# Kernel optimization log

Measured on AMD Instinct MI355X. Metric: run time of the kernel, lower is better.

## Reference

```python
import jax, jax.numpy as jnp
import numpy as np

D0 = 232          # GraphSAGE_TextMF_dyn.model_embedding_dim_origin
NUM_TRAIN = 4096  # num_train_models


def sage_conv(x, edge_index, W_l, b_l, W_r):
    """PyG SAGEConv(aggr='mean'): lin_l(mean_{j in N(i)} x_j) + lin_r(x_i)."""
    src, dst = edge_index[0], edge_index[1]
    msg = x[src]                                                    # [E, Din]
    agg = jax.ops.segment_sum(msg, dst, num_segments=x.shape[0])    # [N, Din]
    deg = jax.ops.segment_sum(jnp.ones((edge_index.shape[1],), x.dtype), dst,
                              num_segments=x.shape[0])
    agg = agg / jnp.maximum(deg, 1.0)[:, None]
    return agg @ W_l.T + b_l + x @ W_r.T


def setup_inputs() -> dict:
    key = jax.random.key(0)
    ks = jax.random.split(key, 12)
    num_models, med, hidden = 5000, 1024, 256
    num_prompts, text_dim = 100000, 768
    B, E = 16384, 131072
    s = lambda d: 1.0 / np.sqrt(d)
    return {
        "P_weight":     jax.random.normal(ks[0], (num_models, med), jnp.float32) * 0.02,
        "model_proj_W": jax.random.normal(ks[1], (D0, med), jnp.float32) * s(med),
        "model_proj_b": jnp.zeros((D0,), jnp.float32),
        "sage1_Wl":     jax.random.normal(ks[2], (hidden, D0), jnp.float32) * s(D0),
        "sage1_bl":     jnp.zeros((hidden,), jnp.float32),
        "sage1_Wr":     jax.random.normal(ks[3], (hidden, D0), jnp.float32) * s(D0),
        "sage2_Wl":     jax.random.normal(ks[4], (D0, hidden), jnp.float32) * s(hidden),
        "sage2_bl":     jnp.zeros((D0,), jnp.float32),
        "sage2_Wr":     jax.random.normal(ks[5], (D0, hidden), jnp.float32) * s(hidden),
        "Q_weight":     jax.random.normal(ks[6], (num_prompts, text_dim), jnp.float32),
        "text_proj_W":  jax.random.normal(ks[7], (D0, text_dim), jnp.float32) * s(text_dim),
        "text_proj_b":  jnp.zeros((D0,), jnp.float32),
        "cls_W":        jax.random.normal(ks[8], (2, D0), jnp.float32) * s(D0),
        "cls_b":        jnp.zeros((2,), jnp.float32),
        "edge_index":   jax.random.randint(ks[9], (2, E), 0, NUM_TRAIN),
        "model_ids":    jax.random.randint(ks[10], (B,), 0, NUM_TRAIN),
        "prompt_ids":   jax.random.randint(ks[11], (B,), 0, num_prompts),
    }


def reference(P_weight, model_proj_W, model_proj_b,
              sage1_Wl, sage1_bl, sage1_Wr,
              sage2_Wl, sage2_bl, sage2_Wr,
              Q_weight, text_proj_W, text_proj_b,
              cls_W, cls_b,
              edge_index, model_ids, prompt_ids):
    # model embedding table -> project to D0
    emb = P_weight @ model_proj_W.T + model_proj_b            # [num_models, D0]
    x = emb[:NUM_TRAIN]                                       # train models only
    # 2-layer GraphSAGE with ReLU between layers
    x = jax.nn.relu(sage_conv(x, edge_index, sage1_Wl, sage1_bl, sage1_Wr))
    x = sage_conv(x, edge_index, sage2_Wl, sage2_bl, sage2_Wr)  # [NUM_TRAIN, D0]
    # TextMF head: classifier(p * q)
    p = x[model_ids]                                          # [B, D0]
    q = Q_weight[prompt_ids] @ text_proj_W.T + text_proj_b    # [B, D0]
    return (p * q) @ cls_W.T + cls_b                          # [B, 2]
```

## Files before the change

### kernel.cpp

```cpp
#include <hip/hip_runtime.h>

#define D0 232
#define MED 1024
#define HID 256
#define TDIM 768
#define NTRAIN 4096

typedef short bf16x8 __attribute__((ext_vector_type(8)));
typedef float f32x4  __attribute__((ext_vector_type(4)));
typedef unsigned short u16;

__device__ __forceinline__ u16 f2bf(float f) {
    unsigned u = __float_as_uint(f);
    return (u16)((u + 0x7FFFu + ((u >> 16) & 1u)) >> 16);
}
__device__ __forceinline__ float bf2f(u16 h) {
    return __uint_as_float(((unsigned)h) << 16);
}
__device__ __forceinline__ void cvt8(const float4& a0, const float4& a1,
                                     bf16x8& h, bf16x8& l) {
    float f[8] = {a0.x, a0.y, a0.z, a0.w, a1.x, a1.y, a1.z, a1.w};
    #pragma unroll
    for (int i = 0; i < 8; ++i) {
        u16 hh = f2bf(f[i]);
        h[i] = (short)hh;
        l[i] = (short)f2bf(f[i] - bf2f(hh));
    }
}

#define SROW(r, k) ((((r) ^ (k)) & 7) | ((r) & ~7))

template<int RELU, int EMIT>
__global__ __launch_bounds__(256) void gemm_node(
    const float* __restrict__ A1,
    const short* __restrict__ Whi, const short* __restrict__ Wlo,
    const short* __restrict__ A2hi, const short* __restrict__ A2lo,
    const short* __restrict__ W2hi, const short* __restrict__ W2lo,
    const float* __restrict__ bias,
    float* __restrict__ Cf, u16* __restrict__ Chi, u16* __restrict__ Clo,
    int M, int N, int K)
{
    constexpr int TBM = 32, TBN = 128;
    __shared__ short sAh[8 * TBM * 8], sAl[8 * TBM * 8];
    __shared__ short sBh[8 * TBN * 8], sBl[8 * TBN * 8];

    const int tid  = threadIdx.x;
    const int lane = tid & 63;
    const int wn   = tid >> 6;
    const int l15  = lane & 15;
    const int l4   = lane >> 4;
    const int row0 = blockIdx.y * TBM;
    const int col0 = blockIdx.x * TBN;

    const int aRow  = tid >> 3;
    const int aKc   = tid & 7;
    const int aSlot = (aKc * TBM + SROW(aRow, aKc)) * 8;

    int bKcA[4], bSlot[4], bRowL[4];
    #pragma unroll
    for (int i = 0; i < 4; ++i) {
        int cid  = tid * 4 + i;
        bRowL[i] = cid >> 3;
        bKcA[i]  = cid & 7;
        bSlot[i] = (bKcA[i] * TBN + SROW(bRowL[i], bKcA[i])) * 8;
    }

    const bf16x8 Z8 = {0, 0, 0, 0, 0, 0, 0, 0};
    f32x4 acc[2][2];
    #pragma unroll
    for (int m = 0; m < 2; ++m)
        #pragma unroll
        for (int j = 0; j < 2; ++j)
            acc[m][j] = (f32x4){0.f, 0.f, 0.f, 0.f};

    for (int pass = 0; pass < 2; ++pass) {
        if (pass && A2hi == nullptr) break;
        const short* Bh = pass ? W2hi : Whi;
        const short* Bl = pass ? W2lo : Wlo;

        const size_t aBase = (size_t)(row0 + aRow) * K;
        size_t bBase[4]; bool bOk[4];
        #pragma unroll
        for (int i = 0; i < 4; ++i) {
            int c = col0 + bRowL[i];
            bOk[i]   = c < N;
            bBase[i] = (size_t)(bOk[i] ? c : 0) * K;
        }

        float4 a0, a1;
        bf16x8 pAh, pAl, rBh[4], rBl[4];

        auto loadT = [&](int k0) {
            int gk = k0 + aKc * 8;
            bool av = gk < K;
            if (pass == 0) {
                a0 = av ? *reinterpret_cast<const float4*>(A1 + aBase + gk)
                        : make_float4(0.f, 0.f, 0.f, 0.f);
                a1 = av ? *reinterpret_cast<const float4*>(A1 + aBase + gk + 4)
                        : make_float4(0.f, 0.f, 0.f, 0.f);
            } else {
                pAh = av ? *reinterpret_cast<const bf16x8*>(A2hi + aBase + gk) : Z8;
                pAl = av ? *reinterpret_cast<const bf16x8*>(A2lo + aBase + gk) : Z8;
            }
            #pragma unroll
            for (int i = 0; i < 4; ++i) {
                int k = k0 + bKcA[i] * 8;
                bool v = bOk[i] && k < K;
                rBh[i] = v ? *reinterpret_cast<const bf16x8*>(Bh + bBase[i] + k) : Z8;
                rBl[i] = v ? *reinterpret_cast<const bf16x8*>(Bl + bBase[i] + k) : Z8;
            }
        };
        auto storeT = [&]() {
            if (pass == 0) {
                bf16x8 h, l; cvt8(a0, a1, h, l);
                *reinterpret_cast<bf16x8*>(sAh + aSlot) = h;
                *reinterpret_cast<bf16x8*>(sAl + aSlot) = l;
            } else {
                *reinterpret_cast<bf16x8*>(sAh + aSlot) = pAh;
                *reinterpret_cast<bf16x8*>(sAl + aSlot) = pAl;
            }
            #pragma unroll
            for (int i = 0; i < 4; ++i) {
                *reinterpret_cast<bf16x8*>(sBh + bSlot[i]) = rBh[i];
                *reinterpret_cast<bf16x8*>(sBl + bSlot[i]) = rBl[i];
            }
        };

        loadT(0);
        for (int k0 = 0; k0 < K; k0 += 64) {
            storeT();
            __syncthreads();
            if (k0 + 64 < K) loadT(k0 + 64);
            #pragma unroll
            for (int ks = 0; ks < 2; ++ks) {
                const int pb = ks * 4 + l4;
                bf16x8 ah[2], al[2], bh[2], bl[2];
                #pragma unroll
                for (int m = 0; m < 2; ++m) {
                    int r  = m * 16 + l15;
                    int sl = (pb * TBM + SROW(r, pb)) * 8;
                    ah[m] = *reinterpret_cast<const bf16x8*>(sAh + sl);
                    al[m] = *reinterpret_cast<const bf16x8*>(sAl + sl);
                }
                #pragma unroll
                for (int j = 0; j < 2; ++j) {
                    int r  = wn * 32 + j * 16 + l15;
                    int sl = (pb * TBN + SROW(r, pb)) * 8;
                    bh[j] = *reinterpret_cast<const bf16x8*>(sBh + sl);
                    bl[j] = *reinterpret_cast<const bf16x8*>(sBl + sl);
                }
                #pragma unroll
                for (int m = 0; m < 2; ++m)
                    #pragma unroll
                    for (int j = 0; j < 2; ++j)
                        acc[m][j] = __builtin_amdgcn_mfma_f32_16x16x32_bf16(
                            ah[m], bh[j], acc[m][j], 0, 0, 0);
                #pragma unroll
                for (int m = 0; m < 2; ++m)
                    #pragma unroll
                    for (int j = 0; j < 2; ++j)
                        acc[m][j] = __builtin_amdgcn_mfma_f32_16x16x32_bf16(
                            ah[m], bl[j], acc[m][j], 0, 0, 0);
                #pragma unroll
                for (int m = 0; m < 2; ++m)
                    #pragma unroll
                    for (int j = 0; j < 2; ++j)
                        acc[m][j] = __builtin_amdgcn_mfma_f32_16x16x32_bf16(
                            al[m], bh[j], acc[m][j], 0, 0, 0);
            }
            __syncthreads();
        }
    }

    #pragma unroll
    for (int j = 0; j < 2; ++j) {
        int col = col0 + wn * 32 + j * 16 + l15;
        if (col >= N) continue;
        float bv = bias[col];
        #pragma unroll
        for (int m = 0; m < 2; ++m) {
            #pragma unroll
            for (int r = 0; r < 4; ++r) {
                int row = row0 + m * 16 + l4 * 4 + r;
                float v = acc[m][j][r] + bv;
                if (RELU) v = fmaxf(v, 0.0f);
                size_t idx = (size_t)row * N + col;
                Cf[idx] = v;
                if (EMIT) {
                    u16 h = f2bf(v);
                    Chi[idx] = h;
                    Clo[idx] = f2bf(v - bf2f(h));
                }
            }
        }
    }
}

__global__ __launch_bounds__(512) void gemm_q_head(
    const float* __restrict__ Q,
    const int* __restrict__ prompt_ids,
    const short* __restrict__ Whi, const short* __restrict__ Wlo,
    const float* __restrict__ bias,
    const float* __restrict__ x2f,
    const int* __restrict__ model_ids,
    const float* __restrict__ cls_W, const float* __restrict__ cls_b,
    float* __restrict__ out)
{
    constexpr int TBM = 64, TBN = 256, K = TDIM, N = D0;
    __shared__ short sAh[8 * TBM * 8], sAl[8 * TBM * 8];
    __shared__ short sBh[8 * TBN * 8], sBl[8 * TBN * 8];
    __shared__ float hacc[TBM][2];

    const int tid  = threadIdx.x;
    const int lane = tid & 63;
    const int wave = tid >> 6;
    const int wm   = wave >> 2;
    const int wn   = wave & 3;
    const int l15  = lane & 15;
    const int l4   = lane >> 4;
    const int row0 = blockIdx.x * TBM;

    const int aRow  = tid >> 3;
    const int aKc   = tid & 7;
    const int aSlot = (aKc * TBM + SROW(aRow, aKc)) * 8;
    const size_t aBase = (size_t)prompt_ids[row0 + aRow] * K;

    int bKcA[4], bSlot[4]; bool bOk[4]; size_t bBase[4];
    #pragma unroll
    for (int i = 0; i < 4; ++i) {
        int cid   = tid * 4 + i;
        int br    = cid >> 3;
        bKcA[i]   = cid & 7;
        bSlot[i]  = (bKcA[i] * TBN + SROW(br, bKcA[i])) * 8;
        bOk[i]    = br < N;
        bBase[i]  = (size_t)(bOk[i] ? br : 0) * K;
    }

    const bf16x8 Z8 = {0, 0, 0, 0, 0, 0, 0, 0};
    f32x4 acc[2][4];
    #pragma unroll
    for (int m = 0; m < 2; ++m)
        #pragma unroll
        for (int j = 0; j < 4; ++j)
            acc[m][j] = (f32x4){0.f, 0.f, 0.f, 0.f};

    float4 a0, a1;
    bf16x8 rBh[4], rBl[4];

    auto loadT = [&](int k0) {
        int gk = k0 + aKc * 8;
        a0 = *reinterpret_cast<const float4*>(Q + aBase + gk);
        a1 = *reinterpret_cast<const float4*>(Q + aBase + gk + 4);
        #pragma unroll
        for (int i = 0; i < 4; ++i) {
            int k = k0 + bKcA[i] * 8;
            rBh[i] = bOk[i] ? *reinterpret_cast<const bf16x8*>(Whi + bBase[i] + k) : Z8;
            rBl[i] = bOk[i] ? *reinterpret_cast<const bf16x8*>(Wlo + bBase[i] + k) : Z8;
        }
    };
    auto storeT = [&]() {
        bf16x8 h, l; cvt8(a0, a1, h, l);
        *reinterpret_cast<bf16x8*>(sAh + aSlot) = h;
        *reinterpret_cast<bf16x8*>(sAl + aSlot) = l;
        #pragma unroll
        for (int i = 0; i < 4; ++i) {
            *reinterpret_cast<bf16x8*>(sBh + bSlot[i]) = rBh[i];
            *reinterpret_cast<bf16x8*>(sBl + bSlot[i]) = rBl[i];
        }
    };

    loadT(0);
    for (int k0 = 0; k0 < K; k0 += 64) {
        storeT();
        __syncthreads();
        if (k0 + 64 < K) loadT(k0 + 64);
        #pragma unroll
        for (int ks = 0; ks < 2; ++ks) {
            const int pb = ks * 4 + l4;
            bf16x8 ah[2], al[2], bh[4], bl[4];
            #pragma unroll
            for (int m = 0; m < 2; ++m) {
                int r  = wm * 32 + m * 16 + l15;
                int sl = (pb * TBM + SROW(r, pb)) * 8;
                ah[m] = *reinterpret_cast<const bf16x8*>(sAh + sl);
                al[m] = *reinterpret_cast<const bf16x8*>(sAl + sl);
            }
            #pragma unroll
            for (int j = 0; j < 4; ++j) {
                int r  = wn * 64 + j * 16 + l15;
                int sl = (pb * TBN + SROW(r, pb)) * 8;
                bh[j] = *reinterpret_cast<const bf16x8*>(sBh + sl);
                bl[j] = *reinterpret_cast<const bf16x8*>(sBl + sl);
            }
            #pragma unroll
            for (int m = 0; m < 2; ++m)
                #pragma unroll
                for (int j = 0; j < 4; ++j)
                    acc[m][j] = __builtin_amdgcn_mfma_f32_16x16x32_bf16(
                        ah[m], bh[j], acc[m][j], 0, 0, 0);
            #pragma unroll
            for (int m = 0; m < 2; ++m)
                #pragma unroll
                for (int j = 0; j < 4; ++j)
                    acc[m][j] = __builtin_amdgcn_mfma_f32_16x16x32_bf16(
                        ah[m], bl[j], acc[m][j], 0, 0, 0);
            #pragma unroll
            for (int m = 0; m < 2; ++m)
                #pragma unroll
                for (int j = 0; j < 4; ++j)
                    acc[m][j] = __builtin_amdgcn_mfma_f32_16x16x32_bf16(
                        al[m], bh[j], acc[m][j], 0, 0, 0);
        }
        __syncthreads();
    }

    for (int t = tid; t < TBM * 2; t += 512) ((float*)hacc)[t] = 0.f;
    __syncthreads();

    int mids[2][4];
    #pragma unroll
    for (int m = 0; m < 2; ++m)
        #pragma unroll
        for (int rr = 0; rr < 4; ++rr)
            mids[m][rr] = model_ids[row0 + wm * 32 + m * 16 + l4 * 4 + rr];

    float s[2][4][2] = {};
    #pragma unroll
    for (int j = 0; j < 4; ++j) {
        int col = wn * 64 + j * 16 + l15;
        if (col < N) {
            float w0 = cls_W[col], w1 = cls_W[N + col], bv = bias[col];
            #pragma unroll
            for (int m = 0; m < 2; ++m) {
                #pragma unroll
                for (int rr = 0; rr < 4; ++rr) {
                    float p  = x2f[(size_t)mids[m][rr] * N + col];
                    float pv = (acc[m][j][rr] + bv) * p;
                    s[m][rr][0] += pv * w0;
                    s[m][rr][1] += pv * w1;
                }
            }
        }
    }
    #pragma unroll
    for (int off = 1; off < 16; off <<= 1)
        #pragma unroll
        for (int m = 0; m < 2; ++m)
            #pragma unroll
            for (int rr = 0; rr < 4; ++rr) {
                s[m][rr][0] += __shfl_xor(s[m][rr][0], off);
                s[m][rr][1] += __shfl_xor(s[m][rr][1], off);
            }
    if (l15 == 0) {
        #pragma unroll
        for (int m = 0; m < 2; ++m)
            #pragma unroll
            for (int rr = 0; rr < 4; ++rr) {
                int lr = wm * 32 + m * 16 + l4 * 4 + rr;
                atomicAdd(&hacc[lr][0], s[m][rr][0]);
                atomicAdd(&hacc[lr][1], s[m][rr][1]);
            }
    }
    __syncthreads();
    for (int t = tid; t < TBM; t += 512) {
        out[(size_t)(row0 + t) * 2 + 0] = hacc[t][0] + cls_b[0];
        out[(size_t)(row0 + t) * 2 + 1] = hacc[t][1] + cls_b[1];
    }
}

struct Seg  { const float* src; u16* hi; u16* lo; int n4; };
struct Segs { Seg s[6]; };

__global__ __launch_bounds__(256) void conv_multi(Segs segs, int total4)
{
    int i = blockIdx.x * blockDim.x + threadIdx.x;
    const int stride = gridDim.x * blockDim.x;
    for (; i < total4; i += stride) {
        int k = i, si = 0;
        while (k >= segs.s[si].n4) { k -= segs.s[si].n4; ++si; }
        float4 v = reinterpret_cast<const float4*>(segs.s[si].src)[k];
        float f[4] = {v.x, v.y, v.z, v.w};
        ushort4 h, l;
        u16* hp = (u16*)&h; u16* lp = (u16*)&l;
        #pragma unroll
        for (int c = 0; c < 4; ++c) {
            u16 hh = f2bf(f[c]);
            hp[c] = hh; lp[c] = f2bf(f[c] - bf2f(hh));
        }
        reinterpret_cast<ushort4*>(segs.s[si].hi)[k] = h;
        reinterpret_cast<ushort4*>(segs.s[si].lo)[k] = l;
    }
}

__global__ void hist_kernel(const int* __restrict__ dst, int* __restrict__ hist, int E)
{
    int e = blockIdx.x * blockDim.x + threadIdx.x;
    if (e < E) atomicAdd(&hist[dst[e]], 1);
}

__global__ __launch_bounds__(1024) void scan_kernel(
    const int* __restrict__ hist, int* __restrict__ row_ptr,
    float* __restrict__ invdeg, int E)
{
    __shared__ int s[1024];
    const int t = threadIdx.x;
    int4 c = reinterpret_cast<const int4*>(hist)[t];
    int local = c.x + c.y + c.z + c.w;
    s[t] = local;
    __syncthreads();
    for (int off = 1; off < 1024; off <<= 1) {
        int v = (t >= off) ? s[t - off] : 0;
        __syncthreads();
        s[t] += v;
        __syncthreads();
    }
    int base = s[t] - local;
    row_ptr[4 * t + 0] = base;
    row_ptr[4 * t + 1] = base + c.x;
    row_ptr[4 * t + 2] = base + c.x + c.y;
    row_ptr[4 * t + 3] = base + c.x + c.y + c.z;
    if (t == 1023) row_ptr[4096] = E;
    invdeg[4 * t + 0] = 1.0f / fmaxf((float)c.x, 1.0f);
    invdeg[4 * t + 1] = 1.0f / fmaxf((float)c.y, 1.0f);
    invdeg[4 * t + 2] = 1.0f / fmaxf((float)c.z, 1.0f);
    invdeg[4 * t + 3] = 1.0f / fmaxf((float)c.w, 1.0f);
}

__global__ void scatter_kernel(
    const int* __restrict__ src, const int* __restrict__ dst,
    const int* __restrict__ row_ptr, int* __restrict__ cursor,
    int* __restrict__ csr, int E)
{
    int e = blockIdx.x * blockDim.x + threadIdx.x;
    if (e >= E) return;
    int d = dst[e];
    int pos = atomicAdd(&cursor[d], 1);
    csr[row_ptr[d] + pos] = src[e];
}

__device__ __forceinline__ void add4(float4& a, const float4 b) {
    a.x += b.x; a.y += b.y; a.z += b.z; a.w += b.w;
}

__global__ __launch_bounds__(256) void node_agg(
    const int* __restrict__ row_ptr, const int* __restrict__ csr,
    const float* __restrict__ invdeg,
    const float* __restrict__ x, float* __restrict__ agg, int D)
{
    const int wave = threadIdx.x >> 6;
    const int lane = threadIdx.x & 63;
    const int node = blockIdx.x * 4 + wave;
    const int beg = row_ptr[node], end = row_ptr[node + 1];
    const bool act = lane < (D >> 2);
    const int fo = lane * 4;

    float4 s0 = {0,0,0,0}, s1 = {0,0,0,0}, s2 = {0,0,0,0}, s3 = {0,0,0,0};
    int j = beg;
    for (; j + 3 < end; j += 4) {
        int n0 = csr[j], n1 = csr[j + 1], n2 = csr[j + 2], n3 = csr[j + 3];
        if (act) {
            add4(s0, *reinterpret_cast<const float4*>(&x[(size_t)n0 * D + fo]));
            add4(s1, *reinterpret_cast<const float4*>(&x[(size_t)n1 * D + fo]));
            add4(s2, *reinterpret_cast<const float4*>(&x[(size_t)n2 * D + fo]));
            add4(s3, *reinterpret_cast<const float4*>(&x[(size_t)n3 * D + fo]));
        }
    }
    for (; j < end; ++j) {
        int n = csr[j];
        if (act) add4(s0, *reinterpret_cast<const float4*>(&x[(size_t)n * D + fo]));
    }
    if (act) {
        const float inv = invdeg[node];
        float4 r;
        r.x = (s0.x + s1.x + s2.x + s3.x) * inv;
        r.y = (s0.y + s1.y + s2.y + s3.y) * inv;
        r.z = (s0.z + s1.z + s2.z + s3.z) * inv;
        r.w = (s0.w + s1.w + s2.w + s3.w) * inv;
        *reinterpret_cast<float4*>(&agg[(size_t)node * D + fo]) = r;
    }
}

extern "C" void kernel_launch(void* const* d_in, const int* in_sizes, int n_in,
                              void* d_out, int out_size, void* d_ws, size_t ws_size,
                              hipStream_t stream)
{
    const float* P_weight     = (const float*)d_in[0];
    const float* model_proj_W = (const float*)d_in[1];
    const float* model_proj_b = (const float*)d_in[2];
    const float* sage1_Wl     = (const float*)d_in[3];
    const float* sage1_bl     = (const float*)d_in[4];
    const float* sage1_Wr     = (const float*)d_in[5];
    const float* sage2_Wl     = (const float*)d_in[6];
    const float* sage2_bl     = (const float*)d_in[7];
    const float* sage2_Wr     = (const float*)d_in[8];
    const float* Q_weight     = (const float*)d_in[9];
    const float* text_proj_W  = (const float*)d_in[10];
    const float* text_proj_b  = (const float*)d_in[11];
    const float* cls_W        = (const float*)d_in[12];
    const float* cls_b        = (const float*)d_in[13];
    const int*   edge_index   = (const int*)d_in[14];
    const int*   model_ids    = (const int*)d_in[15];
    const int*   prompt_ids   = (const int*)d_in[16];

    const int E = in_sizes[14] / 2;
    const int B = in_sizes[15];
    const int* srcE = edge_index;
    const int* dstE = edge_index + E;

    const size_t nX0 = (size_t)NTRAIN * D0;
    const size_t nH1 = (size_t)NTRAIN * HID;
    const size_t nWp = (size_t)D0 * MED;
    const size_t nWs = (size_t)HID * D0;
    const size_t nWt = (size_t)D0 * TDIM;
    const size_t nWAll = nWp + 4 * nWs + nWt;

    float* fp  = (float*)d_ws;
    float* x0f = fp;  fp += nX0;
    float* h1f = fp;  fp += nH1;
    float* x2f = fp;  fp += nX0;
    float* agf = fp;  fp += nH1;
    u16* sp  = (u16*)fp;
    u16* x0h = sp;    sp += nX0;
    u16* x0l = sp;    sp += nX0;
    u16* h1h = sp;    sp += nH1;
    u16* h1l = sp;    sp += nH1;
    u16* Wh  = sp;    sp += nWAll;
    u16* Wl  = sp;    sp += nWAll;
    int* ib  = (int*)sp;
    int*   hist    = ib;
    int*   cursor  = ib + 4096;
    int*   row_ptr = ib + 8192;
    float* invdeg  = (float*)(ib + 12304);
    int*   csr     = ib + 16400;

    u16 *Wph = Wh,            *Wpl = Wl;
    u16 *W1lh = Wh + nWp,     *W1ll = Wl + nWp;
    u16 *W1rh = W1lh + nWs,   *W1rl = W1ll + nWs;
    u16 *W2lh = W1rh + nWs,   *W2ll = W1rl + nWs;
    u16 *W2rh = W2lh + nWs,   *W2rl = W2ll + nWs;
    u16 *Wth  = W2rh + nWs,   *Wtl  = W2rl + nWs;

    dim3 blk(256);

    hipMemsetAsync(ib, 0, 8192 * sizeof(int), stream);

    hist_kernel<<<(E + 255) / 256, blk, 0, stream>>>(dstE, hist, E);
    scan_kernel<<<1, 1024, 0, stream>>>(hist, row_ptr, invdeg, E);
    scatter_kernel<<<(E + 255) / 256, blk, 0, stream>>>(srcE, dstE, row_ptr, cursor, csr, E);

    Segs segs;
    segs.s[0] = {model_proj_W, Wph,  Wpl,  (int)(nWp / 4)};
    segs.s[1] = {sage1_Wl,     W1lh, W1ll, (int)(nWs / 4)};
    segs.s[2] = {sage1_Wr,     W1rh, W1rl, (int)(nWs / 4)};
    segs.s[3] = {sage2_Wl,     W2lh, W2ll, (int)(nWs / 4)};
    segs.s[4] = {sage2_Wr,     W2rh, W2rl, (int)(nWs / 4)};
    segs.s[5] = {text_proj_W,  Wth,  Wtl,  (int)(nWt / 4)};
    conv_multi<<<640, blk, 0, stream>>>(segs, (int)(nWAll / 4));

    gemm_node<0, 1><<<dim3(2, NTRAIN / 32), blk, 0, stream>>>(
        P_weight, (const short*)Wph, (const short*)Wpl,
        nullptr, nullptr, nullptr, nullptr,
        model_proj_b, x0f, x0h, x0l, NTRAIN, D0, MED);

    node_agg<<<NTRAIN / 4, blk, 0, stream>>>(row_ptr, csr, invdeg, x0f, agf, D0);

    gemm_node<1, 1><<<dim3(2, NTRAIN / 32), blk, 0, stream>>>(
        agf, (const short*)W1lh, (const short*)W1ll,
        (const short*)x0h, (const short*)x0l,
        (const short*)W1rh, (const short*)W1rl,
        sage1_bl, h1f, h1h, h1l, NTRAIN, HID, D0);

    node_agg<<<NTRAIN / 4, blk, 0, stream>>>(row_ptr, csr, invdeg, h1f, agf, HID);

    gemm_node<0, 0><<<dim3(2, NTRAIN / 32), blk, 0, stream>>>(
        agf, (const short*)W2lh, (const short*)W2ll,
        (const short*)h1h, (const short*)h1l,
        (const short*)W2rh, (const short*)W2rl,
        sage2_bl, x2f, nullptr, nullptr, NTRAIN, D0, HID);

    gemm_q_head<<<B / 64, dim3(512), 0, stream>>>(
        Q_weight, prompt_ids, (const short*)Wth, (const short*)Wtl,
        text_proj_b, x2f, model_ids, cls_W, cls_b, (float*)d_out);
}
```

Baseline: 167.8 us.

## Load GEMM weight fragments directly into registers, fuse hist with weight conversion

The node GEMMs and the Q-head GEMM no longer stage the weight (B) tiles in shared memory. Each wave now loads its bf16 hi/lo weight fragments straight from global memory into registers. The node GEMM tile narrows to 64 columns with more blocks and a 2-blocks-per-CU launch bound, and the Q-head moves to 256 threads with each wave covering all 64 rows. The histogram kernel is merged with the weight-conversion kernel, the cursor memset moves into the scan, and node_agg writes bf16 hi/lo splits directly so the next GEMM skips its conversion. This removes launches, LDS traffic and syncs, at the cost of redundant global weight reads across row blocks and more register pressure.

```diff
diff --git a/kernel.cpp b/kernel.cpp
--- a/kernel.cpp
+++ b/kernel.cpp
@@ -27,22 +27,28 @@
         l[i] = (short)f2bf(f[i] - bf2f(hh));
     }
 }
+__device__ __forceinline__ void cvt4(const float4 v, ushort4& h, ushort4& l) {
+    h.x = f2bf(v.x); l.x = f2bf(v.x - bf2f(h.x));
+    h.y = f2bf(v.y); l.y = f2bf(v.y - bf2f(h.y));
+    h.z = f2bf(v.z); l.z = f2bf(v.z - bf2f(h.z));
+    h.w = f2bf(v.w); l.w = f2bf(v.w - bf2f(h.w));
+}
 
 #define SROW(r, k) ((((r) ^ (k)) & 7) | ((r) & ~7))
 
-template<int RELU, int EMIT>
-__global__ __launch_bounds__(256) void gemm_node(
-    const float* __restrict__ A1,
-    const short* __restrict__ Whi, const short* __restrict__ Wlo,
-    const short* __restrict__ A2hi, const short* __restrict__ A2lo,
-    const short* __restrict__ W2hi, const short* __restrict__ W2lo,
+template<int CONVA, int RELU, int EMIT, int NPASS>
+__global__ __launch_bounds__(256, 2) void gemm_node(
+    const float* __restrict__ A1f,
+    const short* __restrict__ A1h, const short* __restrict__ A1l,
+    const short* __restrict__ B1h, const short* __restrict__ B1l,
+    const short* __restrict__ A2h, const short* __restrict__ A2l,
+    const short* __restrict__ B2h, const short* __restrict__ B2l,
     const float* __restrict__ bias,
     float* __restrict__ Cf, u16* __restrict__ Chi, u16* __restrict__ Clo,
     int M, int N, int K)
 {
-    constexpr int TBM = 32, TBN = 128;
+    constexpr int TBM = 32;
     __shared__ short sAh[8 * TBM * 8], sAl[8 * TBM * 8];
-    __shared__ short sBh[8 * TBN * 8], sBl[8 * TBN * 8];
 
     const int tid  = threadIdx.x;
     const int lane = tid & 63;
@@ -50,141 +56,98 @@
     const int l15  = lane & 15;
     const int l4   = lane >> 4;
     const int row0 = blockIdx.y * TBM;
-    const int col0 = blockIdx.x * TBN;
+    const int col0 = blockIdx.x * 64;
 
     const int aRow  = tid >> 3;
     const int aKc   = tid & 7;
     const int aSlot = (aKc * TBM + SROW(aRow, aKc)) * 8;
 
-    int bKcA[4], bSlot[4], bRowL[4];
-    #pragma unroll
-    for (int i = 0; i < 4; ++i) {
-        int cid  = tid * 4 + i;
-        bRowL[i] = cid >> 3;
-        bKcA[i]  = cid & 7;
-        bSlot[i] = (bKcA[i] * TBN + SROW(bRowL[i], bKcA[i])) * 8;
-    }
+    const int  colW  = col0 + wn * 16 + l15;
+    const bool colOk = colW < N;
+    const size_t wBase = (size_t)(colOk ? colW : 0) * K;
 
     const bf16x8 Z8 = {0, 0, 0, 0, 0, 0, 0, 0};
-    f32x4 acc[2][2];
-    #pragma unroll
-    for (int m = 0; m < 2; ++m)
-        #pragma unroll
-        for (int j = 0; j < 2; ++j)
-            acc[m][j] = (f32x4){0.f, 0.f, 0.f, 0.f};
-
-    for (int pass = 0; pass < 2; ++pass) {
-        if (pass && A2hi == nullptr) break;
-        const short* Bh = pass ? W2hi : Whi;
-        const short* Bl = pass ? W2lo : Wlo;
-
-        const size_t aBase = (size_t)(row0 + aRow) * K;
-        size_t bBase[4]; bool bOk[4];
-        #pragma unroll
-        for (int i = 0; i < 4; ++i) {
-            int c = col0 + bRowL[i];
-            bOk[i]   = c < N;
-            bBase[i] = (size_t)(bOk[i] ? c : 0) * K;
-        }
-
-        float4 a0, a1;
-        bf16x8 pAh, pAl, rBh[4], rBl[4];
-
-        auto loadT = [&](int k0) {
+    f32x4 acc[2];
+    acc[0] = (f32x4){0.f, 0.f, 0.f, 0.f};
+    acc[1] = (f32x4){0.f, 0.f, 0.f, 0.f};
+
+    for (int pass = 0; pass < NPASS; ++pass) {
+        const short* Bh = pass ? B2h : B1h;
+        const short* Bl = pass ? B2l : B1l;
+        const short* Ah = pass ? A2h : A1h;
+        const short* Al = pass ? A2l : A1l;
+        const size_t aOff = (size_t)(row0 + aRow) * K;
+
+        float4 qa0, qa1;
+        bf16x8 ph, pl;
+
+        auto loadA = [&](int k0) {
             int gk = k0 + aKc * 8;
-            bool av = gk < K;
-            if (pass == 0) {
-                a0 = av ? *reinterpret_cast<const float4*>(A1 + aBase + gk)
-                        : make_float4(0.f, 0.f, 0.f, 0.f);
-                a1 = av ? *reinterpret_cast<const float4*>(A1 + aBase + gk + 4)
-                        : make_float4(0.f, 0.f, 0.f, 0.f);
+            bool v = gk < K;
+            if (CONVA && pass == 0) {
+                qa0 = v ? *(const float4*)(A1f + aOff + gk)     : make_float4(0.f,0.f,0.f,0.f);
+                qa1 = v ? *(const float4*)(A1f + aOff + gk + 4) : make_float4(0.f,0.f,0.f,0.f);
             } else {
-                pAh = av ? *reinterpret_cast<const bf16x8*>(A2hi + aBase + gk) : Z8;
-                pAl = av ? *reinterpret_cast<const bf16x8*>(A2lo + aBase + gk) : Z8;
-            }
-            #pragma unroll
-            for (int i = 0; i < 4; ++i) {
-                int k = k0 + bKcA[i] * 8;
-                bool v = bOk[i] && k < K;
-                rBh[i] = v ? *reinterpret_cast<const bf16x8*>(Bh + bBase[i] + k) : Z8;
-                rBl[i] = v ? *reinterpret_cast<const bf16x8*>(Bl + bBase[i] + k) : Z8;
+                ph = v ? *(const bf16x8*)(Ah + aOff + gk) : Z8;
+                pl = v ? *(const bf16x8*)(Al + aOff + gk) : Z8;
             }
         };
-        auto storeT = [&]() {
-            if (pass == 0) {
-                bf16x8 h, l; cvt8(a0, a1, h, l);
-                *reinterpret_cast<bf16x8*>(sAh + aSlot) = h;
-                *reinterpret_cast<bf16x8*>(sAl + aSlot) = l;
+
+        loadA(0);
+        for (int k0 = 0; k0 < K; k0 += 64) {
+            bf16x8 bh[2], bl[2];
+            #pragma unroll
+            for (int ks = 0; ks < 2; ++ks) {
+                int kb = k0 + (ks * 4 + l4) * 8;
+                bool v = colOk && kb < K;
+                bh[ks] = v ? *(const bf16x8*)(Bh + wBase + kb) : Z8;
+                bl[ks] = v ? *(const bf16x8*)(Bl + wBase + kb) : Z8;
+            }
+            if (CONVA && pass == 0) {
+                bf16x8 h, l; cvt8(qa0, qa1, h, l);
+                *(bf16x8*)(sAh + aSlot) = h;
+                *(bf16x8*)(sAl + aSlot) = l;
             } else {
-                *reinterpret_cast<bf16x8*>(sAh + aSlot) = pAh;
-                *reinterpret_cast<bf16x8*>(sAl + aSlot) = pAl;
-            }
-            #pragma unroll
-            for (int i = 0; i < 4; ++i) {
-                *reinterpret_cast<bf16x8*>(sBh + bSlot[i]) = rBh[i];
-                *reinterpret_cast<bf16x8*>(sBl + bSlot[i]) = rBl[i];
-            }
-        };
-
-        loadT(0);
-        for (int k0 = 0; k0 < K; k0 += 64) {
-            storeT();
+                *(bf16x8*)(sAh + aSlot) = ph;
+                *(bf16x8*)(sAl + aSlot) = pl;
+            }
             __syncthreads();
-            if (k0 + 64 < K) loadT(k0 + 64);
+            if (k0 + 64 < K) loadA(k0 + 64);
+
             #pragma unroll
             for (int ks = 0; ks < 2; ++ks) {
                 const int pb = ks * 4 + l4;
-                bf16x8 ah[2], al[2], bh[2], bl[2];
+                bf16x8 ah[2], al[2];
                 #pragma unroll
                 for (int m = 0; m < 2; ++m) {
-                    int r  = m * 16 + l15;
-                    int sl = (pb * TBM + SROW(r, pb)) * 8;
-                    ah[m] = *reinterpret_cast<const bf16x8*>(sAh + sl);
-                    al[m] = *reinterpret_cast<const bf16x8*>(sAl + sl);
+                    int sl = (pb * TBM + SROW(m * 16 + l15, pb)) * 8;
+                    ah[m] = *(const bf16x8*)(sAh + sl);
+                    al[m] = *(const bf16x8*)(sAl + sl);
                 }
                 #pragma unroll
-                for (int j = 0; j < 2; ++j) {
-                    int r  = wn * 32 + j * 16 + l15;
-                    int sl = (pb * TBN + SROW(r, pb)) * 8;
-                    bh[j] = *reinterpret_cast<const bf16x8*>(sBh + sl);
-                    bl[j] = *reinterpret_cast<const bf16x8*>(sBl + sl);
-                }
-                #pragma unroll
                 for (int m = 0; m < 2; ++m)
-                    #pragma unroll
-                    for (int j = 0; j < 2; ++j)
-                        acc[m][j] = __builtin_amdgcn_mfma_f32_16x16x32_bf16(
-                            ah[m], bh[j], acc[m][j], 0, 0, 0);
+                    acc[m] = __builtin_amdgcn_mfma_f32_16x16x32_bf16(ah[m], bh[ks], acc[m], 0, 0, 0);
                 #pragma unroll
                 for (int m = 0; m < 2; ++m)
-                    #pragma unroll
-                    for (int j = 0; j < 2; ++j)
-                        acc[m][j] = __builtin_amdgcn_mfma_f32_16x16x32_bf16(
-                            ah[m], bl[j], acc[m][j], 0, 0, 0);
+                    acc[m] = __builtin_amdgcn_mfma_f32_16x16x32_bf16(ah[m], bl[ks], acc[m], 0, 0, 0);
                 #pragma unroll
                 for (int m = 0; m < 2; ++m)
-                    #pragma unroll
-                    for (int j = 0; j < 2; ++j)
-                        acc[m][j] = __builtin_amdgcn_mfma_f32_16x16x32_bf16(
-                            al[m], bh[j], acc[m][j], 0, 0, 0);
+                    acc[m] = __builtin_amdgcn_mfma_f32_16x16x32_bf16(al[m], bh[ks], acc[m], 0, 0, 0);
             }
             __syncthreads();
         }
     }
 
-    #pragma unroll
-    for (int j = 0; j < 2; ++j) {
-        int col = col0 + wn * 32 + j * 16 + l15;
-        if (col >= N) continue;
-        float bv = bias[col];
+    if (colOk) {
+        const float bv = bias[colW];
         #pragma unroll
         for (int m = 0; m < 2; ++m) {
             #pragma unroll
             for (int r = 0; r < 4; ++r) {
                 int row = row0 + m * 16 + l4 * 4 + r;
-                float v = acc[m][j][r] + bv;
+                float v = acc[m][r] + bv;
                 if (RELU) v = fmaxf(v, 0.0f);
-                size_t idx = (size_t)row * N + col;
+                size_t idx = (size_t)row * N + colW;
                 Cf[idx] = v;
                 if (EMIT) {
                     u16 h = f2bf(v);
@@ -196,148 +159,132 @@
     }
 }
 
-__global__ __launch_bounds__(512) void gemm_q_head(
-    const float* __restrict__ Q,
-    const int* __restrict__ prompt_ids,
-    const short* __restrict__ Whi, const short* __restrict__ Wlo,
+__global__ __launch_bounds__(256) void gemm_q_head(
+    const float* __restrict__ Q, const int* __restrict__ prompt_ids,
+    const short* __restrict__ Wh, const short* __restrict__ Wl,
     const float* __restrict__ bias,
-    const float* __restrict__ x2f,
-    const int* __restrict__ model_ids,
+    const float* __restrict__ x2f, const int* __restrict__ model_ids,
     const float* __restrict__ cls_W, const float* __restrict__ cls_b,
     float* __restrict__ out)
 {
-    constexpr int TBM = 64, TBN = 256, K = TDIM, N = D0;
+    constexpr int TBM = 64, K = TDIM, N = D0;
     __shared__ short sAh[8 * TBM * 8], sAl[8 * TBM * 8];
-    __shared__ short sBh[8 * TBN * 8], sBl[8 * TBN * 8];
     __shared__ float hacc[TBM][2];
 
     const int tid  = threadIdx.x;
     const int lane = tid & 63;
-    const int wave = tid >> 6;
-    const int wm   = wave >> 2;
-    const int wn   = wave & 3;
+    const int wn   = tid >> 6;
     const int l15  = lane & 15;
     const int l4   = lane >> 4;
     const int row0 = blockIdx.x * TBM;
 
-    const int aRow  = tid >> 3;
-    const int aKc   = tid & 7;
-    const int aSlot = (aKc * TBM + SROW(aRow, aKc)) * 8;
-    const size_t aBase = (size_t)prompt_ids[row0 + aRow] * K;
-
-    int bKcA[4], bSlot[4]; bool bOk[4]; size_t bBase[4];
+    const int cid0 = tid * 2, cid1 = tid * 2 + 1;
+    const int r0 = cid0 >> 3, kc0 = cid0 & 7;
+    const int r1 = cid1 >> 3, kc1 = cid1 & 7;
+    const int slot0 = (kc0 * TBM + SROW(r0, kc0)) * 8;
+    const int slot1 = (kc1 * TBM + SROW(r1, kc1)) * 8;
+    const size_t ab0 = (size_t)prompt_ids[row0 + r0] * K;
+    const size_t ab1 = (size_t)prompt_ids[row0 + r1] * K;
+
+    int colW[4]; bool cOk[4]; size_t wB[4];
     #pragma unroll
-    for (int i = 0; i < 4; ++i) {
-        int cid   = tid * 4 + i;
-        int br    = cid >> 3;
-        bKcA[i]   = cid & 7;
-        bSlot[i]  = (bKcA[i] * TBN + SROW(br, bKcA[i])) * 8;
-        bOk[i]    = br < N;
-        bBase[i]  = (size_t)(bOk[i] ? br : 0) * K;
+    for (int j = 0; j < 4; ++j) {
+        colW[j] = wn * 64 + j * 16 + l15;
+        cOk[j]  = colW[j] < N;
+        wB[j]   = (size_t)(cOk[j] ? colW[j] : 0) * K;
     }
 
     const bf16x8 Z8 = {0, 0, 0, 0, 0, 0, 0, 0};
-    f32x4 acc[2][4];
+    f32x4 acc[4][4];
     #pragma unroll
-    for (int m = 0; m < 2; ++m)
+    for (int m = 0; m < 4; ++m)
         #pragma unroll
         for (int j = 0; j < 4; ++j)
             acc[m][j] = (f32x4){0.f, 0.f, 0.f, 0.f};
 
-    float4 a0, a1;
-    bf16x8 rBh[4], rBl[4];
-
-    auto loadT = [&](int k0) {
-        int gk = k0 + aKc * 8;
-        a0 = *reinterpret_cast<const float4*>(Q + aBase + gk);
-        a1 = *reinterpret_cast<const float4*>(Q + aBase + gk + 4);
-        #pragma unroll
-        for (int i = 0; i < 4; ++i) {
-            int k = k0 + bKcA[i] * 8;
-            rBh[i] = bOk[i] ? *reinterpret_cast<const bf16x8*>(Whi + bBase[i] + k) : Z8;
-            rBl[i] = bOk[i] ? *reinterpret_cast<const bf16x8*>(Wlo + bBase[i] + k) : Z8;
-        }
+    float4 qa0, qa1, qa2, qa3;
+    auto loadA = [&](int k0) {
+        qa0 = *(const float4*)(Q + ab0 + k0 + kc0 * 8);
+        qa1 = *(const float4*)(Q + ab0 + k0 + kc0 * 8 + 4);
+        qa2 = *(const float4*)(Q + ab1 + k0 + kc1 * 8);
+        qa3 = *(const float4*)(Q + ab1 + k0 + kc1 * 8 + 4);
     };
-    auto storeT = [&]() {
-        bf16x8 h, l; cvt8(a0, a1, h, l);
-        *reinterpret_cast<bf16x8*>(sAh + aSlot) = h;
-        *reinterpret_cast<bf16x8*>(sAl + aSlot) = l;
-        #pragma unroll
-        for (int i = 0; i < 4; ++i) {
-            *reinterpret_cast<bf16x8*>(sBh + bSlot[i]) = rBh[i];
-            *reinterpret_cast<bf16x8*>(sBl + bSlot[i]) = rBl[i];
-        }
-    };
-
-    loadT(0);
+
+    loadA(0);
     for (int k0 = 0; k0 < K; k0 += 64) {
-        storeT();
+        bf16x8 bh[2][4], bl[2][4];
+        #pragma unroll
+        for (int ks = 0; ks < 2; ++ks) {
+            int kb = k0 + (ks * 4 + l4) * 8;
+            #pragma unroll
+            for (int j = 0; j < 4; ++j) {
+                bh[ks][j] = cOk[j] ? *(const bf16x8*)(Wh + wB[j] + kb) : Z8;
+                bl[ks][j] = cOk[j] ? *(const bf16x8*)(Wl + wB[j] + kb) : Z8;
+            }
+        }
+        {
+            bf16x8 h, l;
+            cvt8(qa0, qa1, h, l);
+            *(bf16x8*)(sAh + slot0) = h; *(bf16x8*)(sAl + slot0) = l;
+            cvt8(qa2, qa3, h, l);
+            *(bf16x8*)(sAh + slot1) = h; *(bf16x8*)(sAl + slot1) = l;
+        }
         __syncthreads();
-        if (k0 + 64 < K) loadT(k0 + 64);
+        if (k0 + 64 < K) loadA(k0 + 64);
+
         #pragma unroll
         for (int ks = 0; ks < 2; ++ks) {
             const int pb = ks * 4 + l4;
-            bf16x8 ah[2], al[2], bh[4], bl[4];
-            #pragma unroll
-            for (int m = 0; m < 2; ++m) {
-                int r  = wm * 32 + m * 16 + l15;
-                int sl = (pb * TBM + SROW(r, pb)) * 8;
-                ah[m] = *reinterpret_cast<const bf16x8*>(sAh + sl);
-                al[m] = *reinterpret_cast<const bf16x8*>(sAl + sl);
-            }
-            #pragma unroll
-            for (int j = 0; j < 4; ++j) {
-                int r  = wn * 64 + j * 16 + l15;
-                int sl = (pb * TBN + SROW(r, pb)) * 8;
-                bh[j] = *reinterpret_cast<const bf16x8*>(sBh + sl);
-                bl[j] = *reinterpret_cast<const bf16x8*>(sBl + sl);
-            }
-            #pragma unroll
-            for (int m = 0; m < 2; ++m)
+            bf16x8 ah[4], al[4];
+            #pragma unroll
+            for (int m = 0; m < 4; ++m) {
+                int sl = (pb * TBM + SROW(m * 16 + l15, pb)) * 8;
+                ah[m] = *(const bf16x8*)(sAh + sl);
+                al[m] = *(const bf16x8*)(sAl + sl);
+            }
+            #pragma unroll
+            for (int m = 0; m < 4; ++m)
                 #pragma unroll
                 for (int j = 0; j < 4; ++j)
-                    acc[m][j] = __builtin_amdgcn_mfma_f32_16x16x32_bf16(
-                        ah[m], bh[j], acc[m][j], 0, 0, 0);
-            #pragma unroll
-            for (int m = 0; m < 2; ++m)
+                    acc[m][j] = __builtin_amdgcn_mfma_f32_16x16x32_bf16(ah[m], bh[ks][j], acc[m][j], 0, 0, 0);
+            #pragma unroll
+            for (int m = 0; m < 4; ++m)
                 #pragma unroll
                 for (int j = 0; j < 4; ++j)
-                    acc[m][j] = __builtin_amdgcn_mfma_f32_16x16x32_bf16(
-                        ah[m], bl[j], acc[m][j], 0, 0, 0);
-            #pragma unroll
-            for (int m = 0; m < 2; ++m)
+                    acc[m][j] = __builtin_amdgcn_mfma_f32_16x16x32_bf16(ah[m], bl[ks][j], acc[m][j], 0, 0, 0);
+            #pragma unroll
+            for (int m = 0; m < 4; ++m)
                 #pragma unroll
                 for (int j = 0; j < 4; ++j)
-                    acc[m][j] = __builtin_amdgcn_mfma_f32_16x16x32_bf16(
-                        al[m], bh[j], acc[m][j], 0, 0, 0);
+                    acc[m][j] = __builtin_amdgcn_mfma_f32_16x16x32_bf16(al[m], bh[ks][j], acc[m][j], 0, 0, 0);
         }
         __syncthreads();
     }
 
-    for (int t = tid; t < TBM * 2; t += 512) ((float*)hacc)[t] = 0.f;
+    if (tid < TBM * 2) ((float*)hacc)[tid] = 0.f;
     __syncthreads();
 
-    int mids[2][4];
-    #pragma unroll
-    for (int m = 0; m < 2; ++m)
-        #pragma unroll
-        for (int rr = 0; rr < 4; ++rr)
-            mids[m][rr] = model_ids[row0 + wm * 32 + m * 16 + l4 * 4 + rr];
-
-    float s[2][4][2] = {};
+    float bv[4], w0[4], w1[4];
     #pragma unroll
     for (int j = 0; j < 4; ++j) {
-        int col = wn * 64 + j * 16 + l15;
-        if (col < N) {
-            float w0 = cls_W[col], w1 = cls_W[N + col], bv = bias[col];
-            #pragma unroll
-            for (int m = 0; m < 2; ++m) {
-                #pragma unroll
-                for (int rr = 0; rr < 4; ++rr) {
-                    float p  = x2f[(size_t)mids[m][rr] * N + col];
-                    float pv = (acc[m][j][rr] + bv) * p;
-                    s[m][rr][0] += pv * w0;
-                    s[m][rr][1] += pv * w1;
+        bv[j] = cOk[j] ? bias[colW[j]]      : 0.f;
+        w0[j] = cOk[j] ? cls_W[colW[j]]     : 0.f;
+        w1[j] = cOk[j] ? cls_W[N + colW[j]] : 0.f;
+    }
+
+    float s0[4][4] = {}, s1[4][4] = {};
+    #pragma unroll
+    for (int m = 0; m < 4; ++m) {
+        #pragma unroll
+        for (int rr = 0; rr < 4; ++rr) {
+            const int mid = model_ids[row0 + m * 16 + l4 * 4 + rr];
+            const float* xr = x2f + (size_t)mid * N;
+            #pragma unroll
+            for (int j = 0; j < 4; ++j) {
+                if (cOk[j]) {
+                    float pv = (acc[m][j][rr] + bv[j]) * xr[colW[j]];
+                    s0[m][rr] += pv * w0[j];
+                    s1[m][rr] += pv * w1[j];
                 }
             }
         }
@@ -345,62 +292,56 @@
     #pragma unroll
     for (int off = 1; off < 16; off <<= 1)
         #pragma unroll
-        for (int m = 0; m < 2; ++m)
+        for (int m = 0; m < 4; ++m)
             #pragma unroll
             for (int rr = 0; rr < 4; ++rr) {
-                s[m][rr][0] += __shfl_xor(s[m][rr][0], off);
-                s[m][rr][1] += __shfl_xor(s[m][rr][1], off);
+                s0[m][rr] += __shfl_xor(s0[m][rr], off);
+                s1[m][rr] += __shfl_xor(s1[m][rr], off);
             }
     if (l15 == 0) {
         #pragma unroll
-        for (int m = 0; m < 2; ++m)
+        for (int m = 0; m < 4; ++m)
             #pragma unroll
             for (int rr = 0; rr < 4; ++rr) {
-                int lr = wm * 32 + m * 16 + l4 * 4 + rr;
-                atomicAdd(&hacc[lr][0], s[m][rr][0]);
-                atomicAdd(&hacc[lr][1], s[m][rr][1]);
+                int lr = m * 16 + l4 * 4 + rr;
+                atomicAdd(&hacc[lr][0], s0[m][rr]);
+                atomicAdd(&hacc[lr][1], s1[m][rr]);
             }
     }
     __syncthreads();
-    for (int t = tid; t < TBM; t += 512) {
-        out[(size_t)(row0 + t) * 2 + 0] = hacc[t][0] + cls_b[0];
-        out[(size_t)(row0 + t) * 2 + 1] = hacc[t][1] + cls_b[1];
+    if (tid < TBM * 2) {
+        int r = tid >> 1, c = tid & 1;
+        out[(size_t)(row0 + r) * 2 + c] = hacc[r][c] + cls_b[c];
     }
 }
 
 struct Seg  { const float* src; u16* hi; u16* lo; int n4; };
 struct Segs { Seg s[6]; };
 
-__global__ __launch_bounds__(256) void conv_multi(Segs segs, int total4)
-{
-    int i = blockIdx.x * blockDim.x + threadIdx.x;
-    const int stride = gridDim.x * blockDim.x;
-    for (; i < total4; i += stride) {
-        int k = i, si = 0;
-        while (k >= segs.s[si].n4) { k -= segs.s[si].n4; ++si; }
-        float4 v = reinterpret_cast<const float4*>(segs.s[si].src)[k];
-        float f[4] = {v.x, v.y, v.z, v.w};
-        ushort4 h, l;
-        u16* hp = (u16*)&h; u16* lp = (u16*)&l;
-        #pragma unroll
-        for (int c = 0; c < 4; ++c) {
-            u16 hh = f2bf(f[c]);
-            hp[c] = hh; lp[c] = f2bf(f[c] - bf2f(hh));
-        }
-        reinterpret_cast<ushort4*>(segs.s[si].hi)[k] = h;
-        reinterpret_cast<ushort4*>(segs.s[si].lo)[k] = l;
-    }
-}
-
-__global__ void hist_kernel(const int* __restrict__ dst, int* __restrict__ hist, int E)
-{
-    int e = blockIdx.x * blockDim.x + threadIdx.x;
-    if (e < E) atomicAdd(&hist[dst[e]], 1);
+__global__ __launch_bounds__(256) void hist_conv(
+    const int* __restrict__ dst, int* __restrict__ hist, int E, int HB,
+    Segs segs, int total4)
+{
+    if ((int)blockIdx.x < HB) {
+        int e = blockIdx.x * 256 + threadIdx.x;
+        if (e < E) atomicAdd(&hist[dst[e]], 1);
+    } else {
+        int i = (blockIdx.x - HB) * 256 + threadIdx.x;
+        const int stride = (gridDim.x - HB) * 256;
+        for (; i < total4; i += stride) {
+            int k = i, si = 0;
+            while (k >= segs.s[si].n4) { k -= segs.s[si].n4; ++si; }
+            float4 v = ((const float4*)segs.s[si].src)[k];
+            ushort4 h, l; cvt4(v, h, l);
+            ((ushort4*)segs.s[si].hi)[k] = h;
+            ((ushort4*)segs.s[si].lo)[k] = l;
+        }
+    }
 }
 
 __global__ __launch_bounds__(1024) void scan_kernel(
     const int* __restrict__ hist, int* __restrict__ row_ptr,
-    float* __restrict__ invdeg, int E)
+    float* __restrict__ invdeg, int* __restrict__ cursor, int E)
 {
     __shared__ int s[1024];
     const int t = threadIdx.x;
@@ -424,6 +365,7 @@
     invdeg[4 * t + 1] = 1.0f / fmaxf((float)c.y, 1.0f);
     invdeg[4 * t + 2] = 1.0f / fmaxf((float)c.z, 1.0f);
     invdeg[4 * t + 3] = 1.0f / fmaxf((float)c.w, 1.0f);
+    reinterpret_cast<int4*>(cursor)[t] = make_int4(0, 0, 0, 0);
 }
 
 __global__ void scatter_kernel(
@@ -445,7 +387,7 @@
 __global__ __launch_bounds__(256) void node_agg(
     const int* __restrict__ row_ptr, const int* __restrict__ csr,
     const float* __restrict__ invdeg,
-    const float* __restrict__ x, float* __restrict__ agg, int D)
+    const float* __restrict__ x, u16* __restrict__ agh, u16* __restrict__ agl, int D)
 {
     const int wave = threadIdx.x >> 6;
     const int lane = threadIdx.x & 63;
@@ -459,15 +401,15 @@
     for (; j + 3 < end; j += 4) {
         int n0 = csr[j], n1 = csr[j + 1], n2 = csr[j + 2], n3 = csr[j + 3];
         if (act) {
-            add4(s0, *reinterpret_cast<const float4*>(&x[(size_t)n0 * D + fo]));
-            add4(s1, *reinterpret_cast<const float4*>(&x[(size_t)n1 * D + fo]));
-            add4(s2, *reinterpret_cast<const float4*>(&x[(size_t)n2 * D + fo]));
-            add4(s3, *reinterpret_cast<const float4*>(&x[(size_t)n3 * D + fo]));
+            add4(s0, *(const float4*)(&x[(size_t)n0 * D + fo]));
+            add4(s1, *(const float4*)(&x[(size_t)n1 * D + fo]));
+            add4(s2, *(const float4*)(&x[(size_t)n2 * D + fo]));
+            add4(s3, *(const float4*)(&x[(size_t)n3 * D + fo]));
         }
     }
     for (; j < end; ++j) {
         int n = csr[j];
-        if (act) add4(s0, *reinterpret_cast<const float4*>(&x[(size_t)n * D + fo]));
+        if (act) add4(s0, *(const float4*)(&x[(size_t)n * D + fo]));
     }
     if (act) {
         const float inv = invdeg[node];
@@ -476,7 +418,9 @@
         r.y = (s0.y + s1.y + s2.y + s3.y) * inv;
         r.z = (s0.z + s1.z + s2.z + s3.z) * inv;
         r.w = (s0.w + s1.w + s2.w + s3.w) * inv;
-        *reinterpret_cast<float4*>(&agg[(size_t)node * D + fo]) = r;
+        ushort4 h, l; cvt4(r, h, l);
+        *(ushort4*)(&agh[(size_t)node * D + fo]) = h;
+        *(ushort4*)(&agl[(size_t)node * D + fo]) = l;
     }
 }
 
@@ -518,12 +462,13 @@
     float* x0f = fp;  fp += nX0;
     float* h1f = fp;  fp += nH1;
     float* x2f = fp;  fp += nX0;
-    float* agf = fp;  fp += nH1;
     u16* sp  = (u16*)fp;
     u16* x0h = sp;    sp += nX0;
     u16* x0l = sp;    sp += nX0;
     u16* h1h = sp;    sp += nH1;
     u16* h1l = sp;    sp += nH1;
+    u16* agh = sp;    sp += nH1;
+    u16* agl = sp;    sp += nH1;
     u16* Wh  = sp;    sp += nWAll;
     u16* Wl  = sp;    sp += nWAll;
     int* ib  = (int*)sp;
@@ -542,11 +487,7 @@
 
     dim3 blk(256);
 
-    hipMemsetAsync(ib, 0, 8192 * sizeof(int), stream);
-
-    hist_kernel<<<(E + 255) / 256, blk, 0, stream>>>(dstE, hist, E);
-    scan_kernel<<<1, 1024, 0, stream>>>(hist, row_ptr, invdeg, E);
-    scatter_kernel<<<(E + 255) / 256, blk, 0, stream>>>(srcE, dstE, row_ptr, cursor, csr, E);
+    hipMemsetAsync(hist, 0, 4096 * sizeof(int), stream);
 
     Segs segs;
     segs.s[0] = {model_proj_W, Wph,  Wpl,  (int)(nWp / 4)};
@@ -555,30 +496,37 @@
     segs.s[3] = {sage2_Wl,     W2lh, W2ll, (int)(nWs / 4)};
     segs.s[4] = {sage2_Wr,     W2rh, W2rl, (int)(nWs / 4)};
     segs.s[5] = {text_proj_W,  Wth,  Wtl,  (int)(nWt / 4)};
-    conv_multi<<<640, blk, 0, stream>>>(segs, (int)(nWAll / 4));
-
-    gemm_node<0, 1><<<dim3(2, NTRAIN / 32), blk, 0, stream>>>(
-        P_weight, (const short*)Wph, (const short*)Wpl,
+    const int HB = (E + 255) / 256;
+    hist_conv<<<HB + 512, blk, 0, stream>>>(dstE, hist, E, HB, segs, (int)(nWAll / 4));
+
+    scan_kernel<<<1, 1024, 0, stream>>>(hist, row_ptr, invdeg, cursor, E);
+    scatter_kernel<<<(E + 255) / 256, blk, 0, stream>>>(srcE, dstE, row_ptr, cursor, csr, E);
+
+    gemm_node<1, 0, 1, 1><<<dim3(4, NTRAIN / 32), blk, 0, stream>>>(
+        P_weight, nullptr, nullptr,
+        (const short*)Wph, (const short*)Wpl,
         nullptr, nullptr, nullptr, nullptr,
         model_proj_b, x0f, x0h, x0l, NTRAIN, D0, MED);
 
-    node_agg<<<NTRAIN / 4, blk, 0, stream>>>(row_ptr, csr, invdeg, x0f, agf, D0);
-
-    gemm_node<1, 1><<<dim3(2, NTRAIN / 32), blk, 0, stream>>>(
-        agf, (const short*)W1lh, (const short*)W1ll,
+    node_agg<<<NTRAIN / 4, blk, 0, stream>>>(row_ptr, csr, invdeg, x0f, agh, agl, D0);
+
+    gemm_node<0, 1, 1, 2><<<dim3(4, NTRAIN / 32), blk, 0, stream>>>(
+        nullptr, (const short*)agh, (const short*)agl,
+        (const short*)W1lh, (const short*)W1ll,
         (const short*)x0h, (const short*)x0l,
         (const short*)W1rh, (const short*)W1rl,
         sage1_bl, h1f, h1h, h1l, NTRAIN, HID, D0);
 
-    node_agg<<<NTRAIN / 4, blk, 0, stream>>>(row_ptr, csr, invdeg, h1f, agf, HID);
-
-    gemm_node<0, 0><<<dim3(2, NTRAIN / 32), blk, 0, stream>>>(
-        agf, (const short*)W2lh, (const short*)W2ll,
+    node_agg<<<NTRAIN / 4, blk, 0, stream>>>(row_ptr, csr, invdeg, h1f, agh, agl, HID);
+
+    gemm_node<0, 0, 0, 2><<<dim3(4, NTRAIN / 32), blk, 0, stream>>>(
+        nullptr, (const short*)agh, (const short*)agl,
+        (const short*)W2lh, (const short*)W2ll,
         (const short*)h1h, (const short*)h1l,
         (const short*)W2rh, (const short*)W2rl,
         sage2_bl, x2f, nullptr, nullptr, NTRAIN, D0, HID);
 
-    gemm_q_head<<<B / 64, dim3(512), 0, stream>>>(
+    gemm_q_head<<<B / 64, blk, 0, stream>>>(
         Q_weight, prompt_ids, (const short*)Wth, (const short*)Wtl,
         text_proj_b, x2f, model_ids, cls_W, cls_b, (float*)d_out);
 }
```

After: 168.8 us. About the same (+0.6%).
